# Kernel optimization log

Hardware: AMD Instinct MI355X
Metric: run time of the kernel (lower is better)

Reference implementation:

```python
import jax, jax.numpy as jnp
import numpy as np

N = 100_000      # nodes
M = 200_000      # hyperedges
E = 1_000_000    # incidence pairs
D_IN = 64
HEADS, D_OUT = 8, 16   # linear out = 8*16 = 128


def setup_inputs() -> dict:
    key = jax.random.key(0)
    k = jax.random.split(key, 7)
    X = jax.random.normal(k[0], (N, D_IN), dtype=jnp.float32)
    vertex = jax.random.randint(k[1], (E,), 0, N, dtype=jnp.int32)
    edges = jax.random.randint(k[2], (E,), 0, M, dtype=jnp.int32)
    dege = jax.random.uniform(k[3], (M, 1), dtype=jnp.float32)
    degv = jax.random.uniform(k[4], (N, 1), dtype=jnp.float32)
    W = jax.random.normal(k[5], (D_IN, HEADS * D_OUT), dtype=jnp.float32) / np.sqrt(D_IN)
    b = jax.random.normal(k[6], (HEADS * D_OUT,), dtype=jnp.float32) * 0.01
    return {"X": X, "vertex": vertex, "edges": edges, "dege": dege, "degv": degv, "W": W, "b": b}


def reference(X, vertex, edges, dege, degv, W, b):
    n_nodes = X.shape[0]
    n_edges = dege.shape[0]
    # vertex -> hyperedge aggregation (first_aggregate = 'mean')
    Xve = X[vertex]                                               # [E, D]
    sums = jax.ops.segment_sum(Xve, edges, num_segments=n_edges)  # [M, D]
    counts = jax.ops.segment_sum(jnp.ones((edges.shape[0],), X.dtype), edges, num_segments=n_edges)
    Xe = sums / jnp.maximum(counts, 1.0)[:, None]                 # empty edges -> 0
    Xe = Xe * dege
    # hyperedge -> vertex aggregation (sum)
    Xev = Xe[edges]                                               # [E, D]
    Xv = jax.ops.segment_sum(Xev, vertex, num_segments=n_nodes)   # [N, D]
    Xv = Xv * degv
    # normalize_l2: row norm is computed on a DETACHED tensor in torch
    rownorm = jnp.linalg.norm(jax.lax.stop_gradient(Xv), axis=1, keepdims=True)
    scale = jnp.where(rownorm > 0, 1.0 / rownorm, 0.0)
    Xn = Xv * scale
    return Xn @ W + b
```

## Files before the change

### kernel.cpp

```cpp
#include <hip/hip_runtime.h>


#define DIN 64
#define DOUT 128
#define CH 4096
#define BSHIFT 9
#define FINE 512
#define PAYBITS 18
#define PAYMASK ((1u << PAYBITS) - 1u)
#define XB 256
#define STAGE 8192

typedef float f32x4 __attribute__((ext_vector_type(4)));
typedef short bf16x8 __attribute__((ext_vector_type(8)));

__device__ __forceinline__ unsigned short f2b(float f) {
  unsigned u = __float_as_uint(f);
  u = u + 0x7fffu + ((u >> 16) & 1u);
  return (unsigned short)(u >> 16);
}
__device__ __forceinline__ float b2f(unsigned s) {
  return __uint_as_float(s << 16);
}

__global__ __launch_bounds__(512) void k_p1(
    const int* __restrict__ vertex, const int* __restrict__ edges,
    int* __restrict__ G, const float* __restrict__ X,
    unsigned short* __restrict__ Xb, int* __restrict__ done,
    int E, int BKE, int BK, int NCH, int total4) {
  if (blockIdx.x == 0 && threadIdx.x == 0) *done = 0;
  if (blockIdx.x >= (unsigned)NCH) {
    int xb = blockIdx.x - NCH;
    for (int i = xb * 512 + threadIdx.x; i < total4; i += XB * 512) {
      float4 a = ((const float4*)X)[i];
      ushort4 r;
      r.x = f2b(a.x); r.y = f2b(a.y); r.z = f2b(a.z); r.w = f2b(a.w);
      ((ushort4*)Xb)[i] = r;
    }
    return;
  }
  __shared__ int h[1024];
  for (int i = threadIdx.x; i < BK; i += 512) h[i] = 0;
  __syncthreads();
  int c = blockIdx.x;
  int s = c * CH, e_ = min(E, s + CH);
  int n4 = (e_ - s) >> 2;
  const int4* ep = (const int4*)(edges + s);
  const int4* vp = (const int4*)(vertex + s);
  for (int i = threadIdx.x; i < n4; i += 512) {
    int4 ee = ep[i], vv = vp[i];
    atomicAdd(&h[ee.x >> BSHIFT], 1); atomicAdd(&h[ee.y >> BSHIFT], 1);
    atomicAdd(&h[ee.z >> BSHIFT], 1); atomicAdd(&h[ee.w >> BSHIFT], 1);
    atomicAdd(&h[BKE + (vv.x >> BSHIFT)], 1); atomicAdd(&h[BKE + (vv.y >> BSHIFT)], 1);
    atomicAdd(&h[BKE + (vv.z >> BSHIFT)], 1); atomicAdd(&h[BKE + (vv.w >> BSHIFT)], 1);
  }
  for (int i = s + (n4 << 2) + threadIdx.x; i < e_; i += 512) {
    atomicAdd(&h[edges[i] >> BSHIFT], 1);
    atomicAdd(&h[BKE + (vertex[i] >> BSHIFT)], 1);
  }
  __syncthreads();
  for (int b = threadIdx.x; b < BK; b += 512) G[(size_t)b * NCH + c] = h[b];
}

__global__ __launch_bounds__(256) void k_p1b(
    int* __restrict__ G, int* __restrict__ rowTot, int* __restrict__ bucketBase,
    int* __restrict__ done, int NCH, int BK) {
  int b = blockIdx.x;
  int* row = G + (size_t)b * NCH;
  __shared__ int wsum[4];
  __shared__ int carry;
  __shared__ bool amLast;
  if (threadIdx.x == 0) carry = 0;
  __syncthreads();
  for (int base = 0; base < NCH; base += 256) {
    int i = base + threadIdx.x;
    int v = (i < NCH) ? row[i] : 0;
    int lane = threadIdx.x & 63, wid = threadIdx.x >> 6;
    int inc = v;
    #pragma unroll
    for (int o = 1; o < 64; o <<= 1) {
      int t = __shfl_up(inc, o);
      if (lane >= o) inc += t;
    }
    if (lane == 63) wsum[wid] = inc;
    __syncthreads();
    int woff = carry;
    for (int w = 0; w < wid; ++w) woff += wsum[w];
    int excl = woff + inc - v;
    if (i < NCH) row[i] = excl;
    __syncthreads();
    if (threadIdx.x == 0) carry += wsum[0] + wsum[1] + wsum[2] + wsum[3];
    __syncthreads();
  }
  if (threadIdx.x == 0) {
    rowTot[b] = carry;
    __threadfence();
    amLast = (atomicAdd(done, 1) == gridDim.x - 1);
  }
  __syncthreads();
  if (!amLast) return;

  if (threadIdx.x == 0) carry = 0;
  __syncthreads();
  for (int base = 0; base < BK; base += 256) {
    int i = base + threadIdx.x;
    int v = (i < BK) ? atomicAdd(&rowTot[i], 0) : 0;
    int lane = threadIdx.x & 63, wid = threadIdx.x >> 6;
    int inc = v;
    #pragma unroll
    for (int o = 1; o < 64; o <<= 1) {
      int t = __shfl_up(inc, o);
      if (lane >= o) inc += t;
    }
    if (lane == 63) wsum[wid] = inc;
    __syncthreads();
    int woff = carry;
    for (int w = 0; w < wid; ++w) woff += wsum[w];
    int excl = woff + inc - v;
    if (i < BK) bucketBase[i] = excl;
    __syncthreads();
    if (threadIdx.x == 0) carry += wsum[0] + wsum[1] + wsum[2] + wsum[3];
    __syncthreads();
  }
  if (threadIdx.x == 0) bucketBase[BK] = carry;
}

__global__ __launch_bounds__(512) void p2_scatter(
    const int* __restrict__ vertex, const int* __restrict__ edges,
    const int* __restrict__ G, const int* __restrict__ bucketBase,
    unsigned* __restrict__ temp, int E, int BKE, int BK, int NCH) {
  __shared__ int curs[1024];
  int c = blockIdx.x;
  for (int b = threadIdx.x; b < BK; b += 512)
    curs[b] = bucketBase[b] + G[(size_t)b * NCH + c];
  __syncthreads();
  int s = c * CH, e_ = min(E, s + CH);
  int n4 = (e_ - s) >> 2;
  const int4* ep = (const int4*)(edges + s);
  const int4* vp = (const int4*)(vertex + s);
  for (int i = threadIdx.x; i < n4; i += 512) {
    int4 ee = ep[i], vv = vp[i];
    int p;
    p = atomicAdd(&curs[ee.x >> BSHIFT], 1);
    temp[p] = ((unsigned)(ee.x & (FINE - 1)) << PAYBITS) | (unsigned)vv.x;
    p = atomicAdd(&curs[BKE + (vv.x >> BSHIFT)], 1);
    temp[p] = ((unsigned)(vv.x & (FINE - 1)) << PAYBITS) | (unsigned)ee.x;
    p = atomicAdd(&curs[ee.y >> BSHIFT], 1);
    temp[p] = ((unsigned)(ee.y & (FINE - 1)) << PAYBITS) | (unsigned)vv.y;
    p = atomicAdd(&curs[BKE + (vv.y >> BSHIFT)], 1);
    temp[p] = ((unsigned)(vv.y & (FINE - 1)) << PAYBITS) | (unsigned)ee.y;
    p = atomicAdd(&curs[ee.z >> BSHIFT], 1);
    temp[p] = ((unsigned)(ee.z & (FINE - 1)) << PAYBITS) | (unsigned)vv.z;
    p = atomicAdd(&curs[BKE + (vv.z >> BSHIFT)], 1);
    temp[p] = ((unsigned)(vv.z & (FINE - 1)) << PAYBITS) | (unsigned)ee.z;
    p = atomicAdd(&curs[ee.w >> BSHIFT], 1);
    temp[p] = ((unsigned)(ee.w & (FINE - 1)) << PAYBITS) | (unsigned)vv.w;
    p = atomicAdd(&curs[BKE + (vv.w >> BSHIFT)], 1);
    temp[p] = ((unsigned)(vv.w & (FINE - 1)) << PAYBITS) | (unsigned)ee.w;
  }
  for (int i = s + (n4 << 2) + threadIdx.x; i < e_; i += 512) {
    int e = edges[i], v = vertex[i];
    int pE = atomicAdd(&curs[e >> BSHIFT], 1);
    temp[pE] = ((unsigned)(e & (FINE - 1)) << PAYBITS) | (unsigned)v;
    int pV = atomicAdd(&curs[BKE + (v >> BSHIFT)], 1);
    temp[pV] = ((unsigned)(v & (FINE - 1)) << PAYBITS) | (unsigned)e;
  }
}

__global__ __launch_bounds__(512) void p3_sort(
    const unsigned* __restrict__ temp, const int* __restrict__ bucketBase,
    int* __restrict__ off, int* __restrict__ perm, int BKE, int M, int N) {
  __shared__ int hist[FINE];
  __shared__ int pos[FINE];
  __shared__ int wsum[8];
  __shared__ unsigned pairsS[STAGE];
  int g = blockIdx.x;
  bool isE = g < BKE;
  int gg = isE ? g : g - BKE;
  int keyBase = gg << BSHIFT;
  int cap = isE ? M : N;
  int offBase = (isE ? 0 : M) + keyBase;
  int fineCount = min(FINE, cap - keyBase);
  int pairBase = bucketBase[g], pairEnd = bucketBase[g + 1];
  int cnt = pairEnd - pairBase;
  bool staged = cnt <= STAGE;

  hist[threadIdx.x] = 0;
  __syncthreads();
  if (staged) {
    for (int i = threadIdx.x; i < cnt; i += 512) {
      unsigned p = temp[pairBase + i];
      pairsS[i] = p;
      atomicAdd(&hist[p >> PAYBITS], 1);
    }
  } else {
    for (int i = threadIdx.x; i < cnt; i += 512)
      atomicAdd(&hist[temp[pairBase + i] >> PAYBITS], 1);
  }
  __syncthreads();

  int v = hist[threadIdx.x];
  int lane = threadIdx.x & 63, wid = threadIdx.x >> 6;
  int inc = v;
  #pragma unroll
  for (int o = 1; o < 64; o <<= 1) {
    int t = __shfl_up(inc, o);
    if (lane >= o) inc += t;
  }
  if (lane == 63) wsum[wid] = inc;
  __syncthreads();
  int woff = 0;
  for (int w = 0; w < wid; ++w) woff += wsum[w];
  int excl = woff + inc - v;
  pos[threadIdx.x] = excl;
  __syncthreads();

  if ((int)threadIdx.x < fineCount)
    off[offBase + threadIdx.x] = pairBase + pos[threadIdx.x] + hist[threadIdx.x];
  pos[threadIdx.x] += pairBase;
  __syncthreads();

  if (staged) {
    for (int i = threadIdx.x; i < cnt; i += 512) {
      unsigned p = pairsS[i];
      int q = atomicAdd(&pos[p >> PAYBITS], 1);
      perm[q] = (int)(p & PAYMASK);
    }
  } else {
    for (int i = threadIdx.x; i < cnt; i += 512) {
      unsigned p = temp[pairBase + i];
      int q = atomicAdd(&pos[p >> PAYBITS], 1);
      perm[q] = (int)(p & PAYMASK);
    }
  }
}


__global__ __launch_bounds__(256) void k_edge(
    const unsigned short* __restrict__ Xb, const int* __restrict__ off,
    const int* __restrict__ perm, const float* __restrict__ dege,
    unsigned short* __restrict__ Xe, int M) {
  long long gid = (long long)blockIdx.x * 256 + threadIdx.x;
  int wv = (int)(gid >> 6);
  int lane = threadIdx.x & 63;
  int g = lane >> 3, li = lane & 7;
  int e = wv * 8 + g;
  bool valid = e < M;
  int start = 0, end = 0;
  if (valid) { start = e ? off[e - 1] : 0; end = off[e]; }
  int deg = end - start;
  int myidx = (valid && li < deg) ? perm[start + li] : 0;
  int jmax = min(deg, 8);
  int jw = jmax;
  jw = max(jw, __shfl_xor(jw, 8));
  jw = max(jw, __shfl_xor(jw, 16));
  jw = max(jw, __shfl_xor(jw, 32));
  const uint4* X4 = (const uint4*)Xb;
  float acc[8] = {0.f, 0.f, 0.f, 0.f, 0.f, 0.f, 0.f, 0.f};
  #pragma unroll 4
  for (int j = 0; j < jw; ++j) {
    int v0 = __shfl(myidx, (g << 3) + j);
    if (j < jmax) {
      uint4 a = X4[(size_t)v0 * 8 + li];
      acc[0] += b2f(a.x & 0xffffu); acc[1] += b2f(a.x >> 16);
      acc[2] += b2f(a.y & 0xffffu); acc[3] += b2f(a.y >> 16);
      acc[4] += b2f(a.z & 0xffffu); acc[5] += b2f(a.z >> 16);
      acc[6] += b2f(a.w & 0xffffu); acc[7] += b2f(a.w >> 16);
    }
  }
  for (int j = 8; j < deg; ++j) {
    int v0 = perm[start + j];
    uint4 a = X4[(size_t)v0 * 8 + li];
    acc[0] += b2f(a.x & 0xffffu); acc[1] += b2f(a.x >> 16);
    acc[2] += b2f(a.y & 0xffffu); acc[3] += b2f(a.y >> 16);
    acc[4] += b2f(a.z & 0xffffu); acc[5] += b2f(a.z >> 16);
    acc[6] += b2f(a.w & 0xffffu); acc[7] += b2f(a.w >> 16);
  }
  if (valid) {
    float s = dege[e] / fmaxf((float)deg, 1.0f);
    uint4 r;
    r.x = (unsigned)f2b(acc[0] * s) | ((unsigned)f2b(acc[1] * s) << 16);
    r.y = (unsigned)f2b(acc[2] * s) | ((unsigned)f2b(acc[3] * s) << 16);
    r.z = (unsigned)f2b(acc[4] * s) | ((unsigned)f2b(acc[5] * s) << 16);
    r.w = (unsigned)f2b(acc[6] * s) | ((unsigned)f2b(acc[7] * s) << 16);
    ((uint4*)Xe)[(size_t)e * 8 + li] = r;
  }
}

__global__ __launch_bounds__(256) void k_nodeagg(
    const unsigned short* __restrict__ Xe, const int* __restrict__ off,
    const int* __restrict__ perm, const float* __restrict__ degv,
    unsigned short* __restrict__ xn, int N, int M) {
  long long gid = (long long)blockIdx.x * 256 + threadIdx.x;
  int wv = (int)(gid >> 6);
  int lane = threadIdx.x & 63;
  int g = lane >> 3, li = lane & 7;
  int node = wv * 8 + g;
  bool valid = node < N;
  int start = 0, end = 0;
  if (valid) { start = off[M + node - 1]; end = off[M + node]; }
  int deg = end - start;
  int my0 = (valid && li < deg) ? perm[start + li] : 0;
  int my1 = (valid && 8 + li < deg) ? perm[start + 8 + li] : 0;
  int jmax0 = min(deg, 8);
  int jmax1 = min(max(deg - 8, 0), 8);
  int jw0 = jmax0, jw1 = jmax1;
  jw0 = max(jw0, __shfl_xor(jw0, 8)); jw1 = max(jw1, __shfl_xor(jw1, 8));
  jw0 = max(jw0, __shfl_xor(jw0, 16)); jw1 = max(jw1, __shfl_xor(jw1, 16));
  jw0 = max(jw0, __shfl_xor(jw0, 32)); jw1 = max(jw1, __shfl_xor(jw1, 32));
  const uint4* Xe4 = (const uint4*)Xe;
  float acc[8] = {0.f, 0.f, 0.f, 0.f, 0.f, 0.f, 0.f, 0.f};
  #pragma unroll 4
  for (int j = 0; j < jw0; ++j) {
    int e0 = __shfl(my0, (g << 3) + j);
    if (j < jmax0) {
      uint4 a = Xe4[(size_t)e0 * 8 + li];
      acc[0] += b2f(a.x & 0xffffu); acc[1] += b2f(a.x >> 16);
      acc[2] += b2f(a.y & 0xffffu); acc[3] += b2f(a.y >> 16);
      acc[4] += b2f(a.z & 0xffffu); acc[5] += b2f(a.z >> 16);
      acc[6] += b2f(a.w & 0xffffu); acc[7] += b2f(a.w >> 16);
    }
  }
  #pragma unroll 4
  for (int j = 0; j < jw1; ++j) {
    int e0 = __shfl(my1, (g << 3) + j);
    if (j < jmax1) {
      uint4 a = Xe4[(size_t)e0 * 8 + li];
      acc[0] += b2f(a.x & 0xffffu); acc[1] += b2f(a.x >> 16);
      acc[2] += b2f(a.y & 0xffffu); acc[3] += b2f(a.y >> 16);
      acc[4] += b2f(a.z & 0xffffu); acc[5] += b2f(a.z >> 16);
      acc[6] += b2f(a.w & 0xffffu); acc[7] += b2f(a.w >> 16);
    }
  }
  for (int j = 16; j < deg; ++j) {
    int e0 = perm[start + j];
    uint4 a = Xe4[(size_t)e0 * 8 + li];
    acc[0] += b2f(a.x & 0xffffu); acc[1] += b2f(a.x >> 16);
    acc[2] += b2f(a.y & 0xffffu); acc[3] += b2f(a.y >> 16);
    acc[4] += b2f(a.z & 0xffffu); acc[5] += b2f(a.z >> 16);
    acc[6] += b2f(a.w & 0xffffu); acc[7] += b2f(a.w >> 16);
  }
  float dv = valid ? degv[node] : 0.f;
  float ss = 0.f;
  #pragma unroll
  for (int i = 0; i < 8; ++i) { acc[i] *= dv; ss += acc[i] * acc[i]; }
  #pragma unroll
  for (int o = 1; o <= 4; o <<= 1) ss += __shfl_xor(ss, o);
  float sc = ss > 0.0f ? 1.0f / sqrtf(ss) : 0.0f;
  if (valid) {
    uint4 r;
    r.x = (unsigned)f2b(acc[0] * sc) | ((unsigned)f2b(acc[1] * sc) << 16);
    r.y = (unsigned)f2b(acc[2] * sc) | ((unsigned)f2b(acc[3] * sc) << 16);
    r.z = (unsigned)f2b(acc[4] * sc) | ((unsigned)f2b(acc[5] * sc) << 16);
    r.w = (unsigned)f2b(acc[6] * sc) | ((unsigned)f2b(acc[7] * sc) << 16);
    ((uint4*)xn)[(size_t)node * 8 + li] = r;
  }
}

#define WPAD 72
__global__ __launch_bounds__(256) void k_linear(
    const unsigned short* __restrict__ xn, const float* __restrict__ W,
    const float* __restrict__ bias, float* __restrict__ out, int N) {
  __shared__ unsigned short Wt[DOUT * WPAD];
  for (int i = threadIdx.x; i < DIN * DOUT; i += 256) {
    int k = i >> 7, c = i & 127;
    Wt[c * WPAD + k] = f2b(W[i]);
  }
  __syncthreads();
  int lane = threadIdx.x & 63;
  int wid = threadIdx.x >> 6;
  int r = lane & 15, h = lane >> 4;

  bf16x8 Bf[8][2];
  #pragma unroll
  for (int c = 0; c < 8; ++c) {
    #pragma unroll
    for (int ks = 0; ks < 2; ++ks) {
      int col = c * 16 + r;
      int k0 = ks * 32 + h * 8;
      Bf[c][ks] = *(const bf16x8*)&Wt[col * WPAD + k0];
    }
  }
  float bcol[8];
  #pragma unroll
  for (int c = 0; c < 8; ++c) bcol[c] = bias[c * 16 + r];

  int strips = (N + 15) >> 4;
  for (int s = blockIdx.x * 4 + wid; s < strips; s += gridDim.x * 4) {
    int row0 = s << 4;
    const unsigned short* xrow = xn + (size_t)(row0 + r) * DIN;
    bf16x8 a0 = *(const bf16x8*)&xrow[h * 8];
    bf16x8 a1 = *(const bf16x8*)&xrow[32 + h * 8];
    #pragma unroll
    for (int c = 0; c < 8; ++c) {
      f32x4 acc = {bcol[c], bcol[c], bcol[c], bcol[c]};
      acc = __builtin_amdgcn_mfma_f32_16x16x32_bf16(a0, Bf[c][0], acc, 0, 0, 0);
      acc = __builtin_amdgcn_mfma_f32_16x16x32_bf16(a1, Bf[c][1], acc, 0, 0, 0);
      #pragma unroll
      for (int q = 0; q < 4; ++q)
        out[(size_t)(row0 + h * 4 + q) * DOUT + c * 16 + r] = acc[q];
    }
  }
}

extern "C" void kernel_launch(void* const* d_in, const int* in_sizes, int n_in,
                              void* d_out, int out_size, void* d_ws, size_t ws_size,
                              hipStream_t stream) {
  const float* X      = (const float*)d_in[0];
  const int*   vertex = (const int*)d_in[1];
  const int*   edges  = (const int*)d_in[2];
  const float* dege   = (const float*)d_in[3];
  const float* degv   = (const float*)d_in[4];
  const float* W      = (const float*)d_in[5];
  const float* b      = (const float*)d_in[6];
  float* out = (float*)d_out;

  int N = in_sizes[0] / DIN;
  int E = in_sizes[1];
  int M = in_sizes[3];

  int NCH = (E + CH - 1) / CH;
  int BKE = (M + FINE - 1) >> BSHIFT;
  int BKV = (N + FINE - 1) >> BSHIFT;
  int BK  = BKE + BKV;

  unsigned short* Xe = (unsigned short*)d_ws;
  unsigned short* Xb = Xe + (size_t)M * DIN;
  int*   off  = (int*)(Xb + (size_t)N * DIN);
  int*   perm = off + (M + N);
  char*  R    = (char*)(perm + 2 * (size_t)E);
  unsigned*       temp = (unsigned*)R;
  unsigned short* xn   = (unsigned short*)R;
  size_t rBytes = (size_t)2 * E * 4;
  size_t xBytes = (size_t)N * DIN * 2;
  char*  R2   = R + (rBytes > xBytes ? rBytes : xBytes);
  int*   G    = (int*)R2;
  int*   rowTot = G + (size_t)BK * NCH;
  int*   bucketBase = rowTot + BK;
  int*   done = bucketBase + BK + 1;

  int total4 = N * DIN / 4;
  k_p1<<<NCH + XB, 512, 0, stream>>>(vertex, edges, G, X, Xb, done,
                                     E, BKE, BK, NCH, total4);
  k_p1b<<<BK, 256, 0, stream>>>(G, rowTot, bucketBase, done, NCH, BK);
  p2_scatter<<<NCH, 512, 0, stream>>>(vertex, edges, G, bucketBase, temp,
                                      E, BKE, BK, NCH);
  p3_sort<<<BK, 512, 0, stream>>>(temp, bucketBase, off, perm, BKE, M, N);

  int edgeBlocks = (M + 31) / 32;
  k_edge<<<edgeBlocks, 256, 0, stream>>>(Xb, off, perm, dege, Xe, M);

  int nodeWaves = (N + 7) / 8;
  int nodeBlocks = (nodeWaves + 3) / 4;
  k_nodeagg<<<nodeBlocks, 256, 0, stream>>>(Xe, off, perm, degv, xn, N, M);

  int strips = (N + 15) >> 4;
  int linBlocks = (strips + 3) / 4;
  k_linear<<<linBlocks, 256, 0, stream>>>(xn, W, b, out, N);
}
```

Measured before the change: 128.7 us.

## Fuse bucket scan and scatter kernels with a device-wide spin flag

```diff
diff --git a/kernel.cpp b/kernel.cpp
--- a/kernel.cpp
+++ b/kernel.cpp
@@ -26,9 +26,9 @@
 __global__ __launch_bounds__(512) void k_p1(
     const int* __restrict__ vertex, const int* __restrict__ edges,
     int* __restrict__ G, const float* __restrict__ X,
-    unsigned short* __restrict__ Xb, int* __restrict__ done,
+    unsigned short* __restrict__ Xb, int* __restrict__ sync,
     int E, int BKE, int BK, int NCH, int total4) {
-  if (blockIdx.x == 0 && threadIdx.x == 0) *done = 0;
+  if (blockIdx.x == 0 && threadIdx.x == 0) { sync[0] = 0; sync[1] = 0; }
   if (blockIdx.x >= (unsigned)NCH) {
     int xb = blockIdx.x - NCH;
     for (int i = xb * 512 + threadIdx.x; i < total4; i += XB * 512) {
@@ -62,77 +62,96 @@
   for (int b = threadIdx.x; b < BK; b += 512) G[(size_t)b * NCH + c] = h[b];
 }
 
-__global__ __launch_bounds__(256) void k_p1b(
+__global__ __launch_bounds__(512) void k_scan_scatter(
+    const int* __restrict__ vertex, const int* __restrict__ edges,
     int* __restrict__ G, int* __restrict__ rowTot, int* __restrict__ bucketBase,
-    int* __restrict__ done, int NCH, int BK) {
-  int b = blockIdx.x;
-  int* row = G + (size_t)b * NCH;
-  __shared__ int wsum[4];
+    int* __restrict__ sync, unsigned* __restrict__ temp,
+    int E, int BKE, int BK, int NCH) {
+  __shared__ int curs[1024];
+  __shared__ int wsum[8];
   __shared__ int carry;
   __shared__ bool amLast;
-  if (threadIdx.x == 0) carry = 0;
-  __syncthreads();
-  for (int base = 0; base < NCH; base += 256) {
-    int i = base + threadIdx.x;
-    int v = (i < NCH) ? row[i] : 0;
-    int lane = threadIdx.x & 63, wid = threadIdx.x >> 6;
-    int inc = v;
-    #pragma unroll
-    for (int o = 1; o < 64; o <<= 1) {
-      int t = __shfl_up(inc, o);
-      if (lane >= o) inc += t;
-    }
-    if (lane == 63) wsum[wid] = inc;
+
+  if (blockIdx.x < (unsigned)BK) {
+    int b = blockIdx.x;
+    int* row = G + (size_t)b * NCH;
+    if (threadIdx.x == 0) carry = 0;
     __syncthreads();
-    int woff = carry;
-    for (int w = 0; w < wid; ++w) woff += wsum[w];
-    int excl = woff + inc - v;
-    if (i < NCH) row[i] = excl;
+    for (int base = 0; base < NCH; base += 512) {
+      int i = base + threadIdx.x;
+      int v = (i < NCH) ? row[i] : 0;
+      int lane = threadIdx.x & 63, wid = threadIdx.x >> 6;
+      int inc = v;
+      #pragma unroll
+      for (int o = 1; o < 64; o <<= 1) {
+        int t = __shfl_up(inc, o);
+        if (lane >= o) inc += t;
+      }
+      if (lane == 63) wsum[wid] = inc;
+      __syncthreads();
+      int woff = carry;
+      for (int w = 0; w < wid; ++w) woff += wsum[w];
+      int excl = woff + inc - v;
+      if (i < NCH) row[i] = excl;
+      __syncthreads();
+      if (threadIdx.x == 0) {
+        int t = 0;
+        #pragma unroll
+        for (int w = 0; w < 8; ++w) t += wsum[w];
+        carry += t;
+      }
+      __syncthreads();
+    }
+    if (threadIdx.x == 0) {
+      rowTot[b] = carry;
+      __threadfence();
+      amLast = (atomicAdd(&sync[0], 1) == BK - 1);
+    }
     __syncthreads();
-    if (threadIdx.x == 0) carry += wsum[0] + wsum[1] + wsum[2] + wsum[3];
+    if (!amLast) return;
+
+    if (threadIdx.x == 0) carry = 0;
     __syncthreads();
-  }
+    for (int base = 0; base < BK; base += 512) {
+      int i = base + threadIdx.x;
+      int v = (i < BK) ? atomicAdd(&rowTot[i], 0) : 0;
+      int lane = threadIdx.x & 63, wid = threadIdx.x >> 6;
+      int inc = v;
+      #pragma unroll
+      for (int o = 1; o < 64; o <<= 1) {
+        int t = __shfl_up(inc, o);
+        if (lane >= o) inc += t;
+      }
+      if (lane == 63) wsum[wid] = inc;
+      __syncthreads();
+      int woff = carry;
+      for (int w = 0; w < wid; ++w) woff += wsum[w];
+      int excl = woff + inc - v;
+      if (i < BK) bucketBase[i] = excl;
+      __syncthreads();
+      if (threadIdx.x == 0) {
+        int t = 0;
+        #pragma unroll
+        for (int w = 0; w < 8; ++w) t += wsum[w];
+        carry += t;
+      }
+      __syncthreads();
+    }
+    if (threadIdx.x == 0) {
+      bucketBase[BK] = carry;
+      __threadfence();
+      atomicExch(&sync[1], 1);
+    }
+    return;
+  }
+
+  int c = blockIdx.x - BK;
   if (threadIdx.x == 0) {
-    rowTot[b] = carry;
-    __threadfence();
-    amLast = (atomicAdd(done, 1) == gridDim.x - 1);
-  }
-  __syncthreads();
-  if (!amLast) return;
-
-  if (threadIdx.x == 0) carry = 0;
-  __syncthreads();
-  for (int base = 0; base < BK; base += 256) {
-    int i = base + threadIdx.x;
-    int v = (i < BK) ? atomicAdd(&rowTot[i], 0) : 0;
-    int lane = threadIdx.x & 63, wid = threadIdx.x >> 6;
-    int inc = v;
-    #pragma unroll
-    for (int o = 1; o < 64; o <<= 1) {
-      int t = __shfl_up(inc, o);
-      if (lane >= o) inc += t;
-    }
-    if (lane == 63) wsum[wid] = inc;
-    __syncthreads();
-    int woff = carry;
-    for (int w = 0; w < wid; ++w) woff += wsum[w];
-    int excl = woff + inc - v;
-    if (i < BK) bucketBase[i] = excl;
-    __syncthreads();
-    if (threadIdx.x == 0) carry += wsum[0] + wsum[1] + wsum[2] + wsum[3];
-    __syncthreads();
-  }
-  if (threadIdx.x == 0) bucketBase[BK] = carry;
-}
-
-__global__ __launch_bounds__(512) void p2_scatter(
-    const int* __restrict__ vertex, const int* __restrict__ edges,
-    const int* __restrict__ G, const int* __restrict__ bucketBase,
-    unsigned* __restrict__ temp, int E, int BKE, int BK, int NCH) {
-  __shared__ int curs[1024];
-  int c = blockIdx.x;
+    while (atomicAdd(&sync[1], 0) == 0) __builtin_amdgcn_s_sleep(16);
+  }
+  __syncthreads();
   for (int b = threadIdx.x; b < BK; b += 512)
-    curs[b] = bucketBase[b] + G[(size_t)b * NCH + c];
+    curs[b] = atomicAdd(&bucketBase[b], 0) + atomicAdd(&G[(size_t)b * NCH + c], 0);
   __syncthreads();
   int s = c * CH, e_ = min(E, s + CH);
   int n4 = (e_ - s) >> 2;
@@ -437,14 +456,14 @@
   int*   G    = (int*)R2;
   int*   rowTot = G + (size_t)BK * NCH;
   int*   bucketBase = rowTot + BK;
-  int*   done = bucketBase + BK + 1;
+  int*   sync = bucketBase + BK + 1;
 
   int total4 = N * DIN / 4;
-  k_p1<<<NCH + XB, 512, 0, stream>>>(vertex, edges, G, X, Xb, done,
+  k_p1<<<NCH + XB, 512, 0, stream>>>(vertex, edges, G, X, Xb, sync,
                                      E, BKE, BK, NCH, total4);
-  k_p1b<<<BK, 256, 0, stream>>>(G, rowTot, bucketBase, done, NCH, BK);
-  p2_scatter<<<NCH, 512, 0, stream>>>(vertex, edges, G, bucketBase, temp,
-                                      E, BKE, BK, NCH);
+  k_scan_scatter<<<BK + NCH, 512, 0, stream>>>(vertex, edges, G, rowTot,
+                                               bucketBase, sync, temp,
+                                               E, BKE, BK, NCH);
   p3_sort<<<BK, 512, 0, stream>>>(temp, bucketBase, off, perm, BKE, M, N);
 
   int edgeBlocks = (M + 31) / 32;
```

New measurement: 150.2 us. 1.17x slower.
